# Performance work log

Hardware: AMD Instinct MI355X
Metric: run time of the kernel (lower is better)

The kernel has to match this reference:

```python
import jax, jax.numpy as jnp
import numpy as np

SEQ, B, IN, H = 512, 256, 300, 256

def setup_inputs() -> dict:
    key = jax.random.key(0)
    ks = jax.random.split(key, 14)
    s = lambda *sh: 1.0 / np.sqrt(sh[0])
    inp = {
        'secuencia': jax.random.normal(ks[0], (SEQ, B, IN), jnp.float32),
        # RNN cell 1 (forward direction)
        'W1x': jax.random.normal(ks[1], (IN, H), jnp.float32) * s(IN),
        'W1h': jax.random.normal(ks[2], (H, H), jnp.float32) * s(H),
        'b1':  jax.random.normal(ks[3], (H,), jnp.float32) * 0.01,
        # RNN cell 2 (backward direction)
        'W2x': jax.random.normal(ks[4], (IN, H), jnp.float32) * s(IN),
        'W2h': jax.random.normal(ks[5], (H, H), jnp.float32) * s(H),
        'b2':  jax.random.normal(ks[6], (H,), jnp.float32) * 0.01,
        # MLP head (weights stored [in, out])
        'fc1_w': jax.random.normal(ks[7], (2 * H, 2 * H), jnp.float32) * s(2 * H),
        'fc1_b': jnp.zeros((2 * H,), jnp.float32),
        'fc2_w': jax.random.normal(ks[8], (2 * H, H), jnp.float32) * s(2 * H),
        'fc2_b': jnp.zeros((H,), jnp.float32),
        'fs_w':  jax.random.normal(ks[9], (H, 1), jnp.float32) * s(H),
        'fs_b':  jnp.zeros((1,), jnp.float32),
    }
    return inp

def _rnn_scan(seq, Wx, Wh, b):
    # seq: [S, B, IN] -> final hidden [B, H]; Elman cell h' = tanh(x Wx + h Wh + b)
    h0 = jnp.zeros((seq.shape[1], Wh.shape[0]), seq.dtype)
    def step(h, x):
        return jnp.tanh(x @ Wx + h @ Wh + b), None
    h_final, _ = jax.lax.scan(step, h0, seq)
    return h_final

def reference(secuencia, W1x, W1h, b1, W2x, W2h, b2,
              fc1_w, fc1_b, fc2_w, fc2_b, fs_w, fs_b):
    h1 = _rnn_scan(secuencia, W1x, W1h, b1)          # forward pass over time
    h2 = _rnn_scan(secuencia[::-1], W2x, W2h, b2)    # reversed pass over time
    h = jnp.concatenate([h1, h2], axis=1)            # [B, 2H]
    x = jax.nn.relu(h @ fc1_w + fc1_b)
    x = jax.nn.relu(x @ fc2_w + fc2_b)
    out = jnp.tanh(x @ fs_w + fs_b)                  # [B, 1]
    return out.squeeze()
```

## Files before the change

### kernel.cpp

```cpp
#include <hip/hip_runtime.h>

#define DI __device__ __forceinline__

typedef float f32x4 __attribute__((ext_vector_type(4)));
typedef float f4    __attribute__((ext_vector_type(4)));
typedef _Float16 h8 __attribute__((ext_vector_type(8)));
typedef _Float16 h4 __attribute__((ext_vector_type(4)));

#define SEQL 512
#define BATCH 256
#define INF 300
#define HID 256
#define N2 512
#define KP 320


DI float ftanh(float x) {
    float e = __builtin_amdgcn_exp2f(x * 2.8853900817779268f);
    return fmaf(-2.0f, __builtin_amdgcn_rcpf(e + 1.0f), 1.0f);
}

__global__ void prep_kernel(const float* __restrict__ W1x, const float* __restrict__ W2x,
                            const float* __restrict__ b1, const float* __restrict__ b2,
                            _Float16* __restrict__ WTs2, float* __restrict__ bcat)
{
    int c = blockIdx.x * 256 + threadIdx.x;
    if (c < 2 * 5 * 2048) {
        int jn = c / (5 * 2048);
        int r = c - jn * (5 * 2048);
        int s = r >> 11, cc = r & 2047;
        int jt = cc >> 7, kk = (cc >> 6) & 1, lg = (cc >> 4) & 3, lj = cc & 15;
        int j = jn * 256 + jt * 16 + lj;
        int k0 = s * 64 + kk * 32 + lg * 8;
        const float* W = (j < HID) ? W1x : W2x;
        int jj = (j < HID) ? j : j - HID;
        h8 v;
#pragma unroll
        for (int i = 0; i < 8; ++i)
            v[i] = (k0 + i < INF) ? (_Float16)W[(k0 + i) * HID + jj] : (_Float16)0.f;
        ((h8*)WTs2)[c] = v;
    }
    if (c < N2) bcat[c] = (c < HID) ? b1[c] : b2[c - HID];
}

__global__ __launch_bounds__(512, 2) void gemm_pre(
    const float* __restrict__ x, const _Float16* __restrict__ WTs2,
    const float* __restrict__ bcat, _Float16* __restrict__ pre3)
{
    __shared__ _Float16 Ab[1024 * 8];
    __shared__ _Float16 Bb[2048 * 8];
    const int tid = threadIdx.x;
    const int w = tid >> 6, l = tid & 63;
    const int lj = l & 15, lg = l >> 4;
    const int bid = blockIdx.x;
    const int xcd = bid & 7;
    const int idx0 = bid >> 3;
    const int jn = idx0 & 1;
    const int bm = xcd * 128 + (idx0 >> 1);
    const size_t m0 = (size_t)bm * 128;
    const int j0b = jn * 256;
    const int wj = (w >> 1) * 64, wm2 = (w & 1) * 64;

    f32x4 acc[4][4];
#pragma unroll
    for (int a = 0; a < 4; ++a)
#pragma unroll
        for (int b = 0; b < 4; ++b) acc[a][b] = f32x4{0.f, 0.f, 0.f, 0.f};

    const _Float16* Wsrc = WTs2 + (size_t)jn * (5 * 2048 * 8);
    const int am = w * 16 + lj;
    const float* xp = x + (m0 + am) * INF;
    const int kAo = lg * 8;
    char* AbC = (char*)Ab;
    char* BbC = (char*)Bb;

    for (int s = 0; s < 5; ++s) {
#pragma unroll
        for (int q = 0; q < 4; ++q) {
            const _Float16* src = Wsrc + ((size_t)s * 2048 + q * 512 + w * 64 + l) * 8;
            _Float16* dst = &Bb[(q * 512 + w * 64) * 8];
            __builtin_amdgcn_global_load_lds(
                (const __attribute__((address_space(1))) void*)src,
                (__attribute__((address_space(3))) void*)dst, 16, 0, 0);
        }
        {
            const int kA = s * 64 + kAo;
            f4 a0 = *(const f4*)(xp + kA);
            f4 a1 = *(const f4*)(xp + kA + 4);
            h8 v0;
#pragma unroll
            for (int i = 0; i < 4; ++i) { v0[i] = (_Float16)a0[i]; v0[4 + i] = (_Float16)a1[i]; }
            h8 v1;
            if (s < 4) {
                f4 b0 = *(const f4*)(xp + kA + 32);
                f4 b1 = *(const f4*)(xp + kA + 36);
#pragma unroll
                for (int i = 0; i < 4; ++i) { v1[i] = (_Float16)b0[i]; v1[4 + i] = (_Float16)b1[i]; }
            } else {
                const int k1 = kA + 32;
#pragma unroll
                for (int i = 0; i < 8; ++i)
                    v1[i] = (k1 + i < INF) ? (_Float16)xp[k1 + i] : (_Float16)0.f;
            }
            *(h8*)(AbC + (w * 128 + l) * 16) = v0;
            *(h8*)(AbC + (w * 128 + 64 + l) * 16) = v1;
        }
        __syncthreads();
#pragma unroll
        for (int kk = 0; kk < 2; ++kk) {
            h8 aw[4], bx[4];
#pragma unroll
            for (int jt = 0; jt < 4; ++jt)
                aw[jt] = *(const h8*)(BbC + ((((wj >> 4) + jt) * 2 + kk) * 1024 + l * 16));
#pragma unroll
            for (int mt = 0; mt < 4; ++mt)
                bx[mt] = *(const h8*)(AbC + ((((wm2 >> 4) + mt) * 2 + kk) * 1024 + l * 16));
#pragma unroll
            for (int jt = 0; jt < 4; ++jt)
#pragma unroll
                for (int mt = 0; mt < 4; ++mt)
                    acc[jt][mt] = __builtin_amdgcn_mfma_f32_16x16x32_f16(aw[jt], bx[mt], acc[jt][mt], 0, 0, 0);
        }
        __syncthreads();
    }
    f4 bias4[4];
#pragma unroll
    for (int jt = 0; jt < 4; ++jt)
        bias4[jt] = *(const f4*)(bcat + j0b + wj + jt * 16 + lg * 4);
    char* prc = (char*)pre3;
#pragma unroll
    for (int jt = 0; jt < 4; ++jt) {
        int slab = (j0b + wj + jt * 16) >> 4;
#pragma unroll
        for (int mt = 0; mt < 4; ++mt) {
            int M = (int)m0 + wm2 + mt * 16;
            size_t byte = (size_t)(M >> 8) * 262144 + (size_t)slab * 8192
                        + (size_t)((M & 255) + lj) * 32 + (size_t)lg * 8;
            h4 o;
#pragma unroll
            for (int i = 0; i < 4; ++i)
                o[i] = (_Float16)(acc[jt][mt][i] + bias4[jt][i]);
            *(h4*)(prc + byte) = o;
        }
    }
}

__global__ __launch_bounds__(512, 2) void rnn_scan(
    const float* __restrict__ W1h, const float* __restrict__ W2h,
    const _Float16* __restrict__ pre3, float* __restrict__ hcat)
{
    __shared__ char hbs[16384];
    char* hbc = hbs;
    const int tid = threadIdx.x;
    const int w = tid >> 6, l = tid & 63;
    const int lj = l & 15, lg = l >> 4;
    const int dir = blockIdx.x & 1;
    const int b0 = (int)(blockIdx.x >> 1) * 16;
    const float* Wh = dir ? W2h : W1h;
    const int j0 = w * 32;
    const int dirOff = dir ? HID : 0;

    h8 afrag[2][8];
#pragma unroll
    for (int jt = 0; jt < 2; ++jt) {
        int jc = j0 + jt * 16 + lj;
#pragma unroll
        for (int kk = 0; kk < 8; ++kk) {
            h8 t;
#pragma unroll
            for (int i = 0; i < 8; ++i) t[i] = (_Float16)Wh[(kk * 32 + lg * 8 + i) * HID + jc];
            afrag[jt][kk] = t;
        }
    }

    const unsigned rb = (unsigned)l * 16;
    const unsigned wb0 = (unsigned)w * 1024 + (unsigned)(lg >> 1) * 256
                       + (unsigned)lj * 16 + (unsigned)(lg & 1) * 8;

    ((h8*)hbs)[tid] = h8{0, 0, 0, 0, 0, 0, 0, 0};
    __syncthreads();

    const long long sb = dir ? -262144LL : 262144LL;
    const char* pp = (const char*)pre3 + (long long)(dir ? (SEQL - 1) : 0) * 262144
                   + (long long)dir * 131072
                   + (long long)w * 16384 + (long long)(b0 + lj) * 32 + lg * 8;
    h4 pA[2], pB[2];
#pragma unroll
    for (int jt = 0; jt < 2; ++jt) pA[jt] = *(const h4*)(pp + jt * 8192);
    pp += sb;
#pragma unroll
    for (int jt = 0; jt < 2; ++jt) pB[jt] = *(const h4*)(pp + jt * 8192);
    pp += sb;

#define RNN_STEP(RB, WB, P, DO_PF)                                                    \
    do {                                                                              \
        h8 bf[8];                                                                     \
        _Pragma("unroll")                                                             \
        for (int kk = 0; kk < 8; ++kk)                                                \
            bf[kk] = *(const h8*)(hbc + (RB) + kk * 1024 + rb);                       \
        f32x4 acc0, acc1;                                                             \
        _Pragma("unroll")                                                             \
        for (int i = 0; i < 4; ++i) { acc0[i] = (float)P[0][i]; acc1[i] = (float)P[1][i]; } \
        if (DO_PF) {                                                                  \
            P[0] = *(const h4*)(pp);                                                  \
            P[1] = *(const h4*)(pp + 8192);                                           \
            pp += sb;                                                                 \
        }                                                                             \
        _Pragma("unroll")                                                             \
        for (int kk = 0; kk < 8; ++kk)                                                \
            acc0 = __builtin_amdgcn_mfma_f32_16x16x32_f16(afrag[0][kk], bf[kk], acc0, 0, 0, 0); \
        h4 o0;                                                                        \
        _Pragma("unroll")                                                             \
        for (int i = 0; i < 4; ++i) o0[i] = (_Float16)ftanh(acc0[i]);                 \
        *(h4*)(hbc + (WB) + wb0) = o0;                                                \
        _Pragma("unroll")                                                             \
        for (int kk = 0; kk < 8; ++kk)                                                \
            acc1 = __builtin_amdgcn_mfma_f32_16x16x32_f16(afrag[1][kk], bf[kk], acc1, 0, 0, 0); \
        h4 o1;                                                                        \
        _Pragma("unroll")                                                             \
        for (int i = 0; i < 4; ++i) o1[i] = (_Float16)ftanh(acc1[i]);                 \
        *(h4*)(hbc + (WB) + wb0 + 512) = o1;                                          \
        __builtin_amdgcn_sched_barrier(0);                                            \
        asm volatile("s_waitcnt lgkmcnt(0)" ::: "memory");                            \
        __builtin_amdgcn_s_barrier();                                                 \
        __builtin_amdgcn_sched_barrier(0);                                            \
    } while (0)

    for (int tp = 0; tp < 255; ++tp) {
        RNN_STEP(0, 8192, pA, 1);
        RNN_STEP(8192, 0, pB, 1);
    }
    RNN_STEP(0, 8192, pA, 0);

    {
        f32x4 acc0, acc1;
#pragma unroll
        for (int i = 0; i < 4; ++i) { acc0[i] = (float)pB[0][i]; acc1[i] = (float)pB[1][i]; }
        h8 bf[8];
#pragma unroll
        for (int kk = 0; kk < 8; ++kk)
            bf[kk] = *(const h8*)(hbc + 8192 + kk * 1024 + rb);
#pragma unroll
        for (int kk = 0; kk < 8; ++kk) {
            acc0 = __builtin_amdgcn_mfma_f32_16x16x32_f16(afrag[0][kk], bf[kk], acc0, 0, 0, 0);
            acc1 = __builtin_amdgcn_mfma_f32_16x16x32_f16(afrag[1][kk], bf[kk], acc1, 0, 0, 0);
        }
        f4 v0, v1;
#pragma unroll
        for (int i = 0; i < 4; ++i) { v0[i] = ftanh(acc0[i]); v1[i] = ftanh(acc1[i]); }
        float* hc = hcat + (size_t)(b0 + lj) * N2 + dirOff + j0 + lg * 4;
        *(f4*)hc = v0;
        *(f4*)(hc + 16) = v1;
    }
#undef RNN_STEP
}

__global__ __launch_bounds__(256) void head_mlp(
    const float* __restrict__ hcat,
    const float* __restrict__ fc1w, const float* __restrict__ fc1b,
    const float* __restrict__ fc2w, const float* __restrict__ fc2b,
    const float* __restrict__ fsw, const float* __restrict__ fsb,
    float* __restrict__ out)
{
    __shared__ float hs[4 * 512];
    __shared__ float y1[4 * 512];
    __shared__ float y2[4 * 256];
    const int tid = threadIdx.x;
    const int b0 = blockIdx.x * 4;
    const int r = tid >> 6;
    const int lane = tid & 63;

#pragma unroll
    for (int c = 0; c < 2; ++c)
        ((f4*)hs)[c * 256 + tid] = ((const f4*)(hcat + (size_t)b0 * N2))[c * 256 + tid];
    __syncthreads();

    {
        const int j0 = lane * 8;
        f4 a0 = *(const f4*)(fc1b + j0);
        f4 a1 = *(const f4*)(fc1b + j0 + 4);
        for (int k = 0; k < 512; ++k) {
            float h = hs[r * 512 + k];
            f4 w0 = *(const f4*)(fc1w + (size_t)k * 512 + j0);
            f4 w1 = *(const f4*)(fc1w + (size_t)k * 512 + j0 + 4);
#pragma unroll
            for (int i = 0; i < 4; ++i) { a0[i] = fmaf(h, w0[i], a0[i]); a1[i] = fmaf(h, w1[i], a1[i]); }
        }
#pragma unroll
        for (int i = 0; i < 4; ++i) {
            y1[r * 512 + j0 + i]     = fmaxf(a0[i], 0.f);
            y1[r * 512 + j0 + 4 + i] = fmaxf(a1[i], 0.f);
        }
    }
    __syncthreads();

    {
        const int j2 = lane * 4;
        f4 a = *(const f4*)(fc2b + j2);
        for (int k = 0; k < 512; ++k) {
            float yv = y1[r * 512 + k];
            f4 w = *(const f4*)(fc2w + (size_t)k * 256 + j2);
#pragma unroll
            for (int i = 0; i < 4; ++i) a[i] = fmaf(yv, w[i], a[i]);
        }
#pragma unroll
        for (int i = 0; i < 4; ++i) y2[r * 256 + j2 + i] = fmaxf(a[i], 0.f);
    }
    __syncthreads();

    {
        float p = 0.f;
#pragma unroll
        for (int u = 0; u < 4; ++u)
            p = fmaf(y2[r * 256 + lane + u * 64], fsw[lane + u * 64], p);
#pragma unroll
        for (int off = 32; off > 0; off >>= 1) p += __shfl_down(p, off);
        if (lane == 0) out[b0 + r] = ftanh(p + fsb[0]);
    }
}

extern "C" void kernel_launch(void* const* d_in, const int* in_sizes, int n_in,
                              void* d_out, int out_size, void* d_ws, size_t ws_size,
                              hipStream_t stream)
{
    const float* x    = (const float*)d_in[0];
    const float* W1x  = (const float*)d_in[1];
    const float* W1h  = (const float*)d_in[2];
    const float* b1   = (const float*)d_in[3];
    const float* W2x  = (const float*)d_in[4];
    const float* W2h  = (const float*)d_in[5];
    const float* b2   = (const float*)d_in[6];
    const float* fc1w = (const float*)d_in[7];
    const float* fc1b = (const float*)d_in[8];
    const float* fc2w = (const float*)d_in[9];
    const float* fc2b = (const float*)d_in[10];
    const float* fsw  = (const float*)d_in[11];
    const float* fsb  = (const float*)d_in[12];

    char* ws = (char*)d_ws;
    size_t off = 0;
    _Float16* WTs2 = (_Float16*)(ws + off); off += (size_t)2 * 5 * 2048 * 8 * sizeof(_Float16);
    float* bcat    = (float*)(ws + off);    off += (size_t)N2 * sizeof(float);
    float* hcat    = (float*)(ws + off);    off += (size_t)BATCH * N2 * sizeof(float);
    _Float16* pre3 = (_Float16*)(ws + off); off += (size_t)SEQL * BATCH * N2 * sizeof(_Float16);
    if (off > ws_size) return;

    prep_kernel<<<80, 256, 0, stream>>>(W1x, W2x, b1, b2, WTs2, bcat);
    gemm_pre<<<2048, 512, 0, stream>>>(x, WTs2, bcat, pre3);
    rnn_scan<<<(BATCH / 16) * 2, 512, 0, stream>>>(W1h, W2h, pre3, hcat);
    head_mlp<<<64, 256, 0, stream>>>(hcat, fc1w, fc1b, fc2w, fc2b, fsw, fsb, (float*)d_out);
}
```

Before: 508.6 us.

## Pre-convert input sequence to fp16 swizzled tiles for direct-to-LDS GEMM loads

Adds a prep_x kernel that converts the fp32 input sequence into fp16, padded and arranged in the exact LDS tile layout. The projection GEMM can then load A tiles with global_load_lds instead of per-thread fp32 loads and conversion. The aim is to cut register and instruction pressure in the GEMM and speed up its staging. The cost is an extra pass over the input: a full read plus an fp16 write of about 84MB, and more workspace. The original path is kept as a fallback when the workspace is too small.

```diff
diff --git a/kernel.cpp b/kernel.cpp
--- a/kernel.cpp
+++ b/kernel.cpp
@@ -12,7 +12,6 @@
 #define INF 300
 #define HID 256
 #define N2 512
-#define KP 320
 
 
 DI float ftanh(float x) {
@@ -43,8 +42,34 @@
     if (c < N2) bcat[c] = (c < HID) ? b1[c] : b2[c - HID];
 }
 
+__global__ __launch_bounds__(256) void prep_x(const float* __restrict__ x,
+                                              _Float16* __restrict__ xh)
+{
+    int flat = blockIdx.x * 256 + threadIdx.x;
+    int c = flat & 1023;
+    int rest = flat >> 10;
+    int s = rest % 5;
+    int bm = rest / 5;
+    int mt = c >> 7, kk = (c >> 6) & 1, l = c & 63;
+    int m = bm * 128 + mt * 16 + (l & 15);
+    int k0 = s * 64 + kk * 32 + (l >> 4) * 8;
+    const float* src = x + (size_t)m * INF + k0;
+    h8 v;
+    if (k0 + 8 <= INF) {
+        f4 a = *(const f4*)src;
+        f4 b = *(const f4*)(src + 4);
+#pragma unroll
+        for (int i = 0; i < 4; ++i) { v[i] = (_Float16)a[i]; v[4 + i] = (_Float16)b[i]; }
+    } else {
+#pragma unroll
+        for (int i = 0; i < 8; ++i)
+            v[i] = (k0 + i < INF) ? (_Float16)src[i] : (_Float16)0.f;
+    }
+    ((h8*)xh)[flat] = v;
+}
+
 __global__ __launch_bounds__(512, 2) void gemm_pre(
-    const float* __restrict__ x, const _Float16* __restrict__ WTs2,
+    const _Float16* __restrict__ xh, const _Float16* __restrict__ WTs2,
     const float* __restrict__ bcat, _Float16* __restrict__ pre3)
 {
     __shared__ _Float16 Ab[1024 * 8];
@@ -68,6 +93,92 @@
         for (int b = 0; b < 4; ++b) acc[a][b] = f32x4{0.f, 0.f, 0.f, 0.f};
 
     const _Float16* Wsrc = WTs2 + (size_t)jn * (5 * 2048 * 8);
+    const _Float16* Xsrc = xh + (size_t)bm * (5 * 1024 * 8);
+    char* AbC = (char*)Ab;
+    char* BbC = (char*)Bb;
+
+    for (int s = 0; s < 5; ++s) {
+#pragma unroll
+        for (int q = 0; q < 4; ++q) {
+            const _Float16* src = Wsrc + ((size_t)s * 2048 + q * 512 + w * 64 + l) * 8;
+            _Float16* dst = &Bb[(q * 512 + w * 64) * 8];
+            __builtin_amdgcn_global_load_lds(
+                (const __attribute__((address_space(1))) void*)src,
+                (__attribute__((address_space(3))) void*)dst, 16, 0, 0);
+        }
+#pragma unroll
+        for (int q = 0; q < 2; ++q) {
+            const _Float16* src = Xsrc + ((size_t)s * 1024 + q * 512 + w * 64 + l) * 8;
+            _Float16* dst = &Ab[(q * 512 + w * 64) * 8];
+            __builtin_amdgcn_global_load_lds(
+                (const __attribute__((address_space(1))) void*)src,
+                (__attribute__((address_space(3))) void*)dst, 16, 0, 0);
+        }
+        __syncthreads();
+#pragma unroll
+        for (int kk = 0; kk < 2; ++kk) {
+            h8 aw[4], bx[4];
+#pragma unroll
+            for (int jt = 0; jt < 4; ++jt)
+                aw[jt] = *(const h8*)(BbC + ((((wj >> 4) + jt) * 2 + kk) * 1024 + l * 16));
+#pragma unroll
+            for (int mt = 0; mt < 4; ++mt)
+                bx[mt] = *(const h8*)(AbC + ((((wm2 >> 4) + mt) * 2 + kk) * 1024 + l * 16));
+#pragma unroll
+            for (int jt = 0; jt < 4; ++jt)
+#pragma unroll
+                for (int mt = 0; mt < 4; ++mt)
+                    acc[jt][mt] = __builtin_amdgcn_mfma_f32_16x16x32_f16(aw[jt], bx[mt], acc[jt][mt], 0, 0, 0);
+        }
+        __syncthreads();
+    }
+    f4 bias4[4];
+#pragma unroll
+    for (int jt = 0; jt < 4; ++jt)
+        bias4[jt] = *(const f4*)(bcat + j0b + wj + jt * 16 + lg * 4);
+    char* prc = (char*)pre3;
+#pragma unroll
+    for (int jt = 0; jt < 4; ++jt) {
+        int slab = (j0b + wj + jt * 16) >> 4;
+#pragma unroll
+        for (int mt = 0; mt < 4; ++mt) {
+            int M = (int)m0 + wm2 + mt * 16;
+            size_t byte = (size_t)(M >> 8) * 262144 + (size_t)slab * 8192
+                        + (size_t)((M & 255) + lj) * 32 + (size_t)lg * 8;
+            h4 o;
+#pragma unroll
+            for (int i = 0; i < 4; ++i)
+                o[i] = (_Float16)(acc[jt][mt][i] + bias4[jt][i]);
+            *(h4*)(prc + byte) = o;
+        }
+    }
+}
+
+__global__ __launch_bounds__(512, 2) void gemm_pre_fb(
+    const float* __restrict__ x, const _Float16* __restrict__ WTs2,
+    const float* __restrict__ bcat, _Float16* __restrict__ pre3)
+{
+    __shared__ _Float16 Ab[1024 * 8];
+    __shared__ _Float16 Bb[2048 * 8];
+    const int tid = threadIdx.x;
+    const int w = tid >> 6, l = tid & 63;
+    const int lj = l & 15, lg = l >> 4;
+    const int bid = blockIdx.x;
+    const int xcd = bid & 7;
+    const int idx0 = bid >> 3;
+    const int jn = idx0 & 1;
+    const int bm = xcd * 128 + (idx0 >> 1);
+    const size_t m0 = (size_t)bm * 128;
+    const int j0b = jn * 256;
+    const int wj = (w >> 1) * 64, wm2 = (w & 1) * 64;
+
+    f32x4 acc[4][4];
+#pragma unroll
+    for (int a = 0; a < 4; ++a)
+#pragma unroll
+        for (int b = 0; b < 4; ++b) acc[a][b] = f32x4{0.f, 0.f, 0.f, 0.f};
+
+    const _Float16* Wsrc = WTs2 + (size_t)jn * (5 * 2048 * 8);
     const int am = w * 16 + lj;
     const float* xp = x + (m0 + am) * INF;
     const int kAo = lg * 8;
@@ -343,10 +454,18 @@
     float* bcat    = (float*)(ws + off);    off += (size_t)N2 * sizeof(float);
     float* hcat    = (float*)(ws + off);    off += (size_t)BATCH * N2 * sizeof(float);
     _Float16* pre3 = (_Float16*)(ws + off); off += (size_t)SEQL * BATCH * N2 * sizeof(_Float16);
-    if (off > ws_size) return;
+    size_t off_base = off;
+    _Float16* xh   = (_Float16*)(ws + off); off += (size_t)1024 * 5 * 1024 * 8 * sizeof(_Float16);
 
     prep_kernel<<<80, 256, 0, stream>>>(W1x, W2x, b1, b2, WTs2, bcat);
-    gemm_pre<<<2048, 512, 0, stream>>>(x, WTs2, bcat, pre3);
+    if (off <= ws_size) {
+        prep_x<<<20480, 256, 0, stream>>>(x, xh);
+        gemm_pre<<<2048, 512, 0, stream>>>(xh, WTs2, bcat, pre3);
+    } else if (off_base <= ws_size) {
+        gemm_pre_fb<<<2048, 512, 0, stream>>>(x, WTs2, bcat, pre3);
+    } else {
+        return;
+    }
     rnn_scan<<<(BATCH / 16) * 2, 512, 0, stream>>>(W1h, W2h, pre3, hcat);
     head_mlp<<<64, 256, 0, stream>>>(hcat, fc1w, fc1b, fc2w, fc2b, fsw, fsb, (float*)d_out);
 }
```

Measured after the change: 527.2 us. 3.7% more time.
